# Performance work log

Measured on AMD Instinct MI355X. Metric: run time of the kernel, lower is better.

## Reference

```python
import jax, jax.numpy as jnp
import numpy as np
from jax import lax

B, C, H, W = 8, 128, 64, 64
S = 4          # patch_size
RED = 16       # SE reduction


def setup_inputs() -> dict:
    key = jax.random.key(0)
    ks = jax.random.split(key, 20)
    f = lambda k, shp, s=1.0: jax.random.normal(k, shp, dtype=jnp.float32) * s
    return {
        "F1": f(ks[0], (B, C, H // 2, W // 2)),
        "F2": f(ks[1], (B, C, H, W)),
        "F3": f(ks[2], (B, C, 2 * H, 2 * W)),
        "conv_w": f(ks[3], (3, C, C, 3, 3), 0.02),
        "conv_b": f(ks[4], (3, C), 0.02),
        "qw": f(ks[5], (3, C, C), 0.05), "qb": f(ks[6], (3, C), 0.02),
        "kw": f(ks[7], (3, C, C), 0.05), "kb": f(ks[8], (3, C), 0.02),
        "vw": f(ks[9], (3, C, C), 0.05), "vb": f(ks[10], (3, C), 0.02),
        "ca1_w": f(ks[11], (3 * C // RED, 3 * C), 0.05), "ca1_b": f(ks[12], (3 * C // RED,), 0.02),
        "ca2_w": f(ks[13], (3 * C, 3 * C // RED), 0.05), "ca2_b": f(ks[14], (3 * C,), 0.02),
        "c3d_w": f(ks[15], (C, C, 3), 0.05), "c3d_b": f(ks[16], (C,), 0.02),
        "out_w": f(ks[17], (C, C), 0.05), "out_b": f(ks[18], (C,), 0.02),
    }


def _conv3x3(x, w, b):
    y = lax.conv_general_dilated(x, w, (1, 1), 'SAME',
                                 dimension_numbers=('NCHW', 'OIHW', 'NCHW'))
    return y + b[None, :, None, None]


def _coarse_attn(x, qw, qb, kw, kb, vw, vb):
    # Block-coarse attention; A is block-constant so we never build HWxHW.
    b, c, h, w = x.shape
    hb, wb = h // S, w // S
    xb = x.reshape(b, c, hb, S, wb, S)
    x_avg = xb.mean((3, 5)).reshape(b, c, hb * wb).transpose(0, 2, 1)  # (B, Nb, C)
    Q = x_avg @ qw.T + qb
    K = x_avg @ kw.T + kb
    A = jax.nn.softmax(jnp.einsum('bnc,bmc->bnm', Q, K) / jnp.sqrt(jnp.float32(c)), axis=-1)
    V = x.transpose(0, 2, 3, 1).reshape(b, h * w, c) @ vw.T + vb       # (B, HW, C)
    Vb = V.reshape(b, hb, S, wb, S, c).sum((2, 4)).reshape(b, hb * wb, c)  # block-summed V
    ob = jnp.einsum('bnm,bmc->bnc', A, Vb)                             # (B, Nb, C)
    out = jnp.broadcast_to(ob.reshape(b, hb, 1, wb, 1, c), (b, hb, S, wb, S, c))
    return out.reshape(b, h, w, c).transpose(0, 3, 1, 2)


def reference(F1, F2, F3, conv_w, conv_b, qw, qb, kw, kb, vw, vb,
              ca1_w, ca1_b, ca2_w, ca2_b, c3d_w, c3d_b, out_w, out_b):
    bsz = F2.shape[0]
    # bilinear upsample (align_corners=False == half-pixel == jax.image.resize)
    F1u = jax.image.resize(F1, F2.shape, method='bilinear')
    # adaptive_avg_pool2d 2H,2W -> H,W is exact 2x2 mean pooling
    F3d = F3.reshape(bsz, C, H, 2, W, 2).mean((3, 5))
    ins = [F1u, F2, F3d]
    processed = [
        _conv3x3(ins[i], conv_w[i], conv_b[i])
        + _coarse_attn(ins[i], qw[i], qb[i], kw[i], kb[i], vw[i], vb[i])
        for i in range(3)
    ]
    cat = jnp.concatenate(processed, axis=1)  # (B, 3C, H, W)
    # SE channel attention
    y = cat.mean((2, 3))
    y = jax.nn.sigmoid(jax.nn.relu(y @ ca1_w.T + ca1_b) @ ca2_w.T + ca2_b)
    wf = cat * y[:, :, None, None]
    # conv3d (3,1,1) pad (1,0,0) then take depth index 1 == full contraction over depth
    stack = jnp.stack((wf[:, :C], wf[:, C:2 * C], wf[:, 2 * C:]), axis=2)  # (B, C, 3, H, W)
    mid = jnp.einsum('ocd,bcdhw->bohw', c3d_w, stack) + c3d_b[None, :, None, None]
    return jnp.einsum('oc,bchw->bohw', out_w, mid) + out_b[None, :, None, None]
```

## Files before the change

kernel.cpp:

```cpp
#include <hip/hip_runtime.h>
#include <hip/hip_bf16.h>
#include <cstddef>


typedef __bf16 bf16x8 __attribute__((ext_vector_type(8)));
typedef float f32x4 __attribute__((ext_vector_type(4)));

__device__ __forceinline__ unsigned short f2bf(float f) {
  unsigned int u = __float_as_uint(f);
  return (unsigned short)((u + 0x7fffu + ((u >> 16) & 1u)) >> 16);
}
__device__ __forceinline__ float bf2f(unsigned short h) {
  return __uint_as_float(((unsigned int)h) << 16);
}
__device__ __forceinline__ unsigned int packbf(float a, float b) {
  return (unsigned int)f2bf(a) | ((unsigned int)f2bf(b) << 16);
}

__global__ __launch_bounds__(256) void k_prep0(
    const float* __restrict__ conv_w, unsigned short* __restrict__ WG,
    const float* __restrict__ qw, const float* __restrict__ kw, const float* __restrict__ vw,
    float* __restrict__ qwT, float* __restrict__ kwT, float* __restrict__ vwT,
    const float* __restrict__ out_w, const float* __restrict__ c3d_w,
    float* __restrict__ comb2, const float* __restrict__ c3d_b,
    const float* __restrict__ out_b, float* __restrict__ fb,
    unsigned short* __restrict__ INS, float* __restrict__ ym,
    const float* __restrict__ F1, const float* __restrict__ F2,
    const float* __restrict__ F3) {
  int blk = blockIdx.x;
  int t = threadIdx.x;
  __shared__ alignas(16) unsigned short L[64 * 136];
  if (blk < 384) {
    int i = blk >> 7, co = blk & 127;
    float* Lw = (float*)L;
    const float* src = conv_w + (size_t)blk * 1152;
    for (int q = t; q < 1152; q += 256) Lw[q] = src[q];
    __syncthreads();
    for (int id = t; id < 576; id += 256) {
      int tap = id >> 6, cp = id & 63;
      int cc = cp >> 4, e = (cp & 15) * 2;
      unsigned int w = packbf(Lw[(cp * 2) * 9 + tap], Lw[(cp * 2 + 1) * 9 + tap]);
      *(unsigned int*)(WG + ((size_t)(((i * 9 + tap) * 4 + cc) * 128 + co)) * 32 + e) = w;
    }
    return;
  } else if (blk < 576) {
    int idx = (blk - 384) * 256 + t;
    int c = idx & 127, k = (idx >> 7) & 127, i = idx >> 14;
    int src = (i * 128 + c) * 128 + k;
    qwT[idx] = qw[src];
    kwT[idx] = kw[src];
    vwT[idx] = vw[src];
    return;
  } else if (blk < 768) {
    int idx = (blk - 576) * 256 + t;
    int j = idx % 384, o = idx / 384;
    int c = j & 127, d = j >> 7;
    float s = 0.f;
    for (int m = 0; m < 128; m++)
      s += out_w[o * 128 + m] * c3d_w[(m * 128 + c) * 3 + d];
    comb2[idx] = s;
    return;
  } else if (blk == 768) {
    if (t < 128) {
      float s = out_b[t];
      for (int m = 0; m < 128; m++) s += out_w[t * 128 + m] * c3d_b[m];
      fb[t] = s;
    }
    for (int z = t; z < 3072; z += 256) ym[z] = 0.f;
    return;
  } else if (blk < 793) {
    int ib = blk - 769;
    uint4 z = {0u, 0u, 0u, 0u};
    for (int id = t; id < 4160; id += 256) {
      int pxI = id >> 4, seg = id & 15;
      int yy, xxp;
      if (pxI < 66) { yy = 0; xxp = pxI; }
      else if (pxI < 132) { yy = 65; xxp = pxI - 66; }
      else if (pxI < 196) { yy = pxI - 131; xxp = 0; }
      else { yy = pxI - 195; xxp = 65; }
      *(uint4*)(INS + (((size_t)ib * 66 + yy) * 66 + xxp) * 128 + seg * 8) = z;
    }
    return;
  }
  int pidx = blk - 793;
  int y = pidx & 63, b = (pidx >> 6) & 7, i = pidx >> 9;
  int ib = i * 8 + b;
  if (i == 1) {
    int x = t & 63, cg = t >> 6;
    unsigned short* lrow = L + x * 136 + cg * 32;
    const float* src = F2 + (((size_t)b * 128 + cg * 32) * 64 + y) * 64 + x;
#pragma unroll 4
    for (int k = 0; k < 32; k += 2) {
      float a = src[(size_t)k * 4096];
      float c = src[(size_t)(k + 1) * 4096];
      *(unsigned int*)(lrow + k) = packbf(a, c);
    }
  } else if (i == 2) {
    int xp = t & 31, cg8 = t >> 5;
    const float* src = F3 + (((size_t)b * 128 + cg8 * 16) * 128 + 2 * y) * 128 + 4 * xp;
    unsigned short* l0 = L + (2 * xp) * 136 + cg8 * 16;
    unsigned short* l1 = L + (2 * xp + 1) * 136 + cg8 * 16;
#pragma unroll
    for (int k = 0; k < 16; ++k) {
      const float* p = src + (size_t)k * 16384;
      float4 a = *(const float4*)p;
      float4 c = *(const float4*)(p + 128);
      l0[k] = f2bf(0.25f * (a.x + a.y + c.x + c.y));
      l1[k] = f2bf(0.25f * (a.z + a.w + c.z + c.w));
    }
  } else {
    int x = t & 63, cg = t >> 6;
    unsigned short* lrow = L + x * 136 + cg * 32;
    int ky = y >> 1, kx = x >> 1;
    int y0, y1, x0, x1;
    float wy0, wx0;
    if (y & 1) { y0 = ky; y1 = (ky + 1 < 32) ? ky + 1 : 31; wy0 = 0.75f; }
    else       { y0 = (ky - 1 > 0) ? ky - 1 : 0; y1 = ky;   wy0 = 0.25f; }
    if (x & 1) { x0 = kx; x1 = (kx + 1 < 32) ? kx + 1 : 31; wx0 = 0.75f; }
    else       { x0 = (kx - 1 > 0) ? kx - 1 : 0; x1 = kx;   wx0 = 0.25f; }
    const float* base = F1 + ((size_t)b * 128 + cg * 32) * 1024;
#pragma unroll 4
    for (int k = 0; k < 32; k += 2) {
      float v[2];
#pragma unroll
      for (int kk = 0; kk < 2; ++kk) {
        const float* p = base + (size_t)(k + kk) * 1024;
        float top = wx0 * p[y0 * 32 + x0] + (1.f - wx0) * p[y0 * 32 + x1];
        float bot = wx0 * p[y1 * 32 + x0] + (1.f - wx0) * p[y1 * 32 + x1];
        v[kk] = wy0 * top + (1.f - wy0) * bot;
      }
      *(unsigned int*)(lrow + k) = packbf(v[0], v[1]);
    }
  }
  __syncthreads();
  unsigned short* dst = INS + (((size_t)ib * 66 + (y + 1)) * 66 + 1) * 128;
#pragma unroll
  for (int q = 0; q < 4; ++q) {
    int id = t + 256 * q;
    int xx = id >> 4, cseg = id & 15;
    uint4 v = *(const uint4*)(&L[xx * 136 + cseg * 8]);
    *(uint4*)(dst + (size_t)id * 8) = v;
  }
}

__global__ __launch_bounds__(256) void k_qkv(
    const unsigned short* __restrict__ INS,
    const float* __restrict__ qwT, const float* __restrict__ qb,
    const float* __restrict__ kwT, const float* __restrict__ kb,
    const float* __restrict__ vwT, const float* __restrict__ vb,
    unsigned short* __restrict__ Qb, unsigned short* __restrict__ Km,
    unsigned short* __restrict__ VT) {
  int nc = blockIdx.x, b = blockIdx.y, i = blockIdx.z;
  int ib = i * 8 + b;
  int t = threadIdx.x;
  __shared__ float xs[16 * 128];
  {
    int n = t >> 4, cs = t & 15;
    int gn = nc * 16 + n;
    int by = gn >> 4, bx = gn & 15;
    float acc[8];
#pragma unroll
    for (int e = 0; e < 8; ++e) acc[e] = 0.f;
#pragma unroll
    for (int ry = 0; ry < 4; ++ry) {
      int y = by * 4 + ry;
      const unsigned short* row = INS + (((size_t)ib * 66 + y + 1) * 66 + 1) * 128 + cs * 8;
#pragma unroll
      for (int rx = 0; rx < 4; ++rx) {
        int x = bx * 4 + rx;
        uint4 v0 = *(const uint4*)(row + (size_t)x * 128);
        unsigned int u[4] = {v0.x, v0.y, v0.z, v0.w};
#pragma unroll
        for (int q = 0; q < 4; ++q) {
          acc[2 * q] += bf2f((unsigned short)(u[q] & 0xffffu));
          acc[2 * q + 1] += bf2f((unsigned short)(u[q] >> 16));
        }
      }
    }
#pragma unroll
    for (int e = 0; e < 8; ++e) xs[n * 128 + cs * 8 + e] = acc[e] * (1.f / 16.f);
  }
  __syncthreads();
  int c = t & 127, nh = t >> 7;
  float aq[8], ak[8], av[8];
#pragma unroll
  for (int z = 0; z < 8; z++) { aq[z] = 0.f; ak[z] = 0.f; av[z] = 0.f; }
  for (int k = 0; k < 128; ++k) {
    float wq = qwT[(i * 128 + k) * 128 + c];
    float wk = kwT[(i * 128 + k) * 128 + c];
    float wv = vwT[(i * 128 + k) * 128 + c];
#pragma unroll
    for (int nn = 0; nn < 8; ++nn) {
      float xv = xs[(nh * 8 + nn) * 128 + k];
      aq[nn] += xv * wq; ak[nn] += xv * wk; av[nn] += xv * wv;
    }
  }
  float bq = qb[i * 128 + c], bk = kb[i * 128 + c], bv = vb[i * 128 + c];
  alignas(16) unsigned short vt[8];
#pragma unroll
  for (int nn = 0; nn < 8; ++nn) {
    size_t row = ((size_t)(ib * 256 + nc * 16 + nh * 8 + nn)) * 128 + c;
    Qb[row] = f2bf(aq[nn] + bq);
    Km[row] = f2bf(ak[nn] + bk);
    vt[nn] = f2bf(16.f * (av[nn] + bv));
  }
  *(uint4*)(VT + ((size_t)(ib * 128 + c)) * 256 + nc * 16 + nh * 8) = *(uint4*)vt;
}

__global__ __launch_bounds__(256) void k_attn(
    const unsigned short* __restrict__ Qb, const unsigned short* __restrict__ K,
    const unsigned short* __restrict__ VT, float* __restrict__ OB) {
  int nc = blockIdx.x, b = blockIdx.y, i = blockIdx.z;
  int ib = i * 8 + b;
  int qbase = nc * 16;
  int t = threadIdx.x;
  int w = t >> 6, l = t & 63;
  int lr = l & 15, lk = (l >> 4) * 8;
  __shared__ float Ss[16 * 260];
  __shared__ alignas(16) unsigned short Pb[16 * 280];

  const float SC = 0.08838834764831845f;
  {
    bf16x8 aq[4];
#pragma unroll
    for (int ks = 0; ks < 4; ++ks)
      aq[ks] = *(const bf16x8*)(Qb + ((size_t)(ib * 256 + qbase + lr)) * 128 + ks * 32 + lk);
    f32x4 acc[4];
#pragma unroll
    for (int nt = 0; nt < 4; ++nt) acc[nt] = {0.f, 0.f, 0.f, 0.f};
#pragma unroll
    for (int ks = 0; ks < 4; ++ks)
#pragma unroll
      for (int nt = 0; nt < 4; ++nt) {
        bf16x8 bk = *(const bf16x8*)(K + ((size_t)(ib * 256 + w * 64 + nt * 16 + lr)) * 128 + ks * 32 + lk);
        acc[nt] = __builtin_amdgcn_mfma_f32_16x16x32_bf16(aq[ks], bk, acc[nt], 0, 0, 0);
      }
#pragma unroll
    for (int nt = 0; nt < 4; ++nt)
#pragma unroll
      for (int r = 0; r < 4; ++r)
        Ss[((l >> 4) * 4 + r) * 260 + w * 64 + nt * 16 + lr] = acc[nt][r] * SC;
  }
  __syncthreads();
  {
    int n = t >> 4, ms = t & 15;
    float vals[16];
    float mx = -1e30f;
#pragma unroll
    for (int j = 0; j < 16; ++j) { vals[j] = Ss[n * 260 + ms + 16 * j]; mx = fmaxf(mx, vals[j]); }
    for (int d = 1; d < 16; d <<= 1) mx = fmaxf(mx, __shfl_xor(mx, d));
    float sum = 0.f;
#pragma unroll
    for (int j = 0; j < 16; ++j) { vals[j] = __expf(vals[j] - mx); sum += vals[j]; }
    for (int d = 1; d < 16; d <<= 1) sum += __shfl_xor(sum, d);
    float inv = 1.f / sum;
#pragma unroll
    for (int j = 0; j < 16; ++j) Pb[n * 280 + ms + 16 * j] = f2bf(vals[j] * inv);
  }
  __syncthreads();
  {
    f32x4 acc[2];
    acc[0] = {0.f, 0.f, 0.f, 0.f};
    acc[1] = acc[0];
#pragma unroll
    for (int ks = 0; ks < 8; ++ks) {
      bf16x8 ap = *(const bf16x8*)(&Pb[lr * 280 + ks * 32 + lk]);
#pragma unroll
      for (int nt = 0; nt < 2; ++nt) {
        bf16x8 bv = *(const bf16x8*)(VT + ((size_t)(ib * 128 + w * 32 + nt * 16 + lr)) * 256 + ks * 32 + lk);
        acc[nt] = __builtin_amdgcn_mfma_f32_16x16x32_bf16(ap, bv, acc[nt], 0, 0, 0);
      }
    }
#pragma unroll
    for (int nt = 0; nt < 2; ++nt)
#pragma unroll
      for (int r = 0; r < 4; ++r) {
        int q = (l >> 4) * 4 + r;
        int ch = w * 32 + nt * 16 + lr;
        OB[((size_t)(ib * 256 + qbase + q)) * 128 + ch] = acc[nt][r];
      }
  }
}

__global__ __launch_bounds__(256) void k_conv(
    const unsigned short* __restrict__ INS, const unsigned short* __restrict__ WG,
    const float* __restrict__ conv_b, const float* __restrict__ OB,
    unsigned short* __restrict__ catT, float* __restrict__ Ysum) {
  int yr = blockIdx.x;
  int yp = ((yr & 7) << 2) | (yr >> 3);
  int y0 = yp * 2;
  int b = blockIdx.y, i = blockIdx.z;
  int ib = i * 8 + b;
  int t = threadIdx.x;
  __shared__ alignas(16) unsigned short smem[17408];
  int w = t >> 6, l = t & 63;
  int lr = l & 15, q4 = l >> 4;

  f32x4 acc[2][2][4];
#pragma unroll
  for (int ro = 0; ro < 2; ++ro)
#pragma unroll
    for (int s = 0; s < 2; s++)
#pragma unroll
      for (int p = 0; p < 4; p++) acc[ro][s][p] = 0.f;

  auto stageX = [&](int h) {
    for (int cI = t; cI < 2112; cI += 256) {
      int seg = cI & 7, rj = cI >> 3;
      int r = rj / 66, j = rj - r * 66;
      uint4 v = *(const uint4*)(INS + (((size_t)ib * 66 + y0 + r) * 66 + j) * 128 + h * 64 + seg * 8);
      *(uint4*)(&smem[(r * 66 + j) * 64 + ((seg ^ (j & 7)) * 8)]) = v;
    }
  };

  const unsigned short* wbase = WG + (size_t)(i * 9) * 4 * 128 * 32 + (w * 32 + lr) * 32 + q4 * 8;
  auto wload = [&](bf16x8* dst, int s) {
    int tap = s % 9, cc = s / 9;
    const unsigned short* wp = wbase + (size_t)(tap * 4 + cc) * 4096;
    dst[0] = *(const bf16x8*)(wp);
    dst[1] = *(const bf16x8*)(wp + 16 * 32);
  };
  bf16x8 wbuf[3][2];
  stageX(0);
  wload(wbuf[0], 0);
  wload(wbuf[1], 1);
  __syncthreads();

#pragma unroll
  for (int s = 0; s < 36; ++s) {
    if (s + 2 < 36) wload(wbuf[(s + 2) % 3], s + 2);
    int tap = s % 9;
    int cc2 = (s / 9) & 1;
    int dy = tap / 3, dx = tap - dy * 3;
    int sid = cc2 * 4 + q4;
#pragma unroll
    for (int ro = 0; ro < 2; ++ro) {
      bf16x8 bfv[4];
#pragma unroll
      for (int p = 0; p < 4; ++p) {
        int j = p * 16 + lr + dx;
        bfv[p] = *(const bf16x8*)(&smem[((dy + ro) * 66 + j) * 64 + ((sid ^ (j & 7)) * 8)]);
      }
#pragma unroll
      for (int sf = 0; sf < 2; ++sf)
#pragma unroll
        for (int p = 0; p < 4; ++p)
          acc[ro][sf][p] = __builtin_amdgcn_mfma_f32_16x16x32_bf16(wbuf[s % 3][sf], bfv[p], acc[ro][sf][p], 0, 0, 0);
    }
    if (s == 17) {
      __syncthreads();
      stageX(1);
      __syncthreads();
    }
  }
  __syncthreads();

  unsigned short* Tt = smem;
  int cobase[2];
  cobase[0] = w * 32 + q4 * 4;
  cobase[1] = w * 32 + 16 + q4 * 4;
  float cb[2][4], ys[2][4];
#pragma unroll
  for (int sf = 0; sf < 2; ++sf)
#pragma unroll
    for (int q = 0; q < 4; ++q) {
      cb[sf][q] = conv_b[i * 128 + cobase[sf] + q];
      ys[sf][q] = 0.f;
    }
#pragma unroll
  for (int ro = 0; ro < 2; ++ro) {
    int nbase = ((y0 + ro) >> 2) * 16;
#pragma unroll
    for (int sf = 0; sf < 2; ++sf) {
#pragma unroll
      for (int p = 0; p < 4; ++p) {
        int px = p * 16 + lr;
        int n = nbase + (px >> 2);
        float4 obv = *(const float4*)(OB + ((size_t)(ib * 256 + n)) * 128 + cobase[sf]);
        float v0 = acc[ro][sf][p][0] + cb[sf][0] + obv.x;
        float v1 = acc[ro][sf][p][1] + cb[sf][1] + obv.y;
        float v2 = acc[ro][sf][p][2] + cb[sf][2] + obv.z;
        float v3 = acc[ro][sf][p][3] + cb[sf][3] + obv.w;
        ys[sf][0] += v0; ys[sf][1] += v1; ys[sf][2] += v2; ys[sf][3] += v3;
        int ploc = ro * 64 + px;
        *(unsigned int*)(&Tt[ploc * 136 + cobase[sf]]) = packbf(v0, v1);
        *(unsigned int*)(&Tt[ploc * 136 + cobase[sf] + 2]) = packbf(v2, v3);
      }
    }
  }
#pragma unroll
  for (int sf = 0; sf < 2; ++sf)
#pragma unroll
    for (int q = 0; q < 4; ++q) {
      float r = ys[sf][q];
      r += __shfl_xor(r, 1);
      r += __shfl_xor(r, 2);
      r += __shfl_xor(r, 4);
      r += __shfl_xor(r, 8);
      if (lr == 0) atomicAdd(&Ysum[b * 384 + i * 128 + cobase[sf] + q], r);
    }
  __syncthreads();
  for (int c2 = t; c2 < 2048; c2 += 256) {
    int ploc = c2 >> 4, seg = c2 & 15;
    uint4 v = *(const uint4*)(&Tt[ploc * 136 + seg * 8]);
    int yy = y0 + (ploc >> 6), xx = ploc & 63;
    *(uint4*)(catT + (((size_t)b * 4096) + yy * 64 + xx) * 384 + i * 128 + seg * 8) = v;
  }
}

__global__ __launch_bounds__(256) void k_final(
    const float* __restrict__ Ysum,
    const float* __restrict__ ca1_w, const float* __restrict__ ca1_b,
    const float* __restrict__ ca2_w, const float* __restrict__ ca2_b,
    const float* __restrict__ comb2, const unsigned short* __restrict__ catT,
    const float* __restrict__ fb, float* __restrict__ out) {
  int pc = blockIdx.x, b = blockIdx.y;
  int t = threadIdx.x;
  __shared__ alignas(16) unsigned short fsm[20480];
  __shared__ float ysh[384];
  __shared__ float sig[384];
  __shared__ float z1[24];
  unsigned short* Ab0 = fsm;
  unsigned short* Ab1 = fsm + 5120;
  unsigned short* Bb0 = fsm + 10240;
  unsigned short* Bb1 = fsm + 15360;

  int w = t >> 6, l = t & 63;
  int wo = w >> 1, wp = w & 1;
  int lr = l & 15, lk = (l >> 4) * 8;

  for (int j = t; j < 384; j += 256) ysh[j] = Ysum[b * 384 + j] * (1.f / 4096.f);
  __syncthreads();
  if (t < 24) {
    float s = ca1_b[t];
    for (int k = 0; k < 384; k++) s += ca1_w[t * 384 + k] * ysh[k];
    z1[t] = fmaxf(s, 0.f);
  }
  __syncthreads();
  for (int j = t; j < 384; j += 256) {
    float s = ca2_b[j];
#pragma unroll
    for (int k = 0; k < 24; k++) s += ca2_w[j * 24 + k] * z1[k];
    sig[j] = 1.f / (1.f + __expf(-s));
  }
  __syncthreads();

  f32x4 acc[4][4];
#pragma unroll
  for (int s = 0; s < 4; s++)
#pragma unroll
    for (int p = 0; p < 4; p++) acc[s][p] = 0.f;

  auto stageA = [&](unsigned short* Adst, int c) {
#pragma unroll
    for (int q = 0; q < 2; ++q) {
      int id = t + 256 * q;
      int o = id >> 2, seg = id & 3;
      int jb = c * 32 + seg * 8;
      const float* src = comb2 + (size_t)o * 384 + jb;
      float4 a = *(const float4*)src;
      float4 b4 = *(const float4*)(src + 4);
      alignas(16) unsigned short tmp[8];
      tmp[0] = f2bf(a.x * sig[jb + 0]);
      tmp[1] = f2bf(a.y * sig[jb + 1]);
      tmp[2] = f2bf(a.z * sig[jb + 2]);
      tmp[3] = f2bf(a.w * sig[jb + 3]);
      tmp[4] = f2bf(b4.x * sig[jb + 4]);
      tmp[5] = f2bf(b4.y * sig[jb + 5]);
      tmp[6] = f2bf(b4.z * sig[jb + 6]);
      tmp[7] = f2bf(b4.w * sig[jb + 7]);
      *(uint4*)(&Adst[o * 40 + seg * 8]) = *(uint4*)tmp;
    }
  };

  stageA(Ab0, 0);
  for (int q = 0; q < 2; ++q) {
    int id = t + 256 * q;
    int o = id >> 2, seg = id & 3;
    uint4 vb = *(const uint4*)(catT + ((size_t)b * 4096 + pc * 128 + o) * 384 + seg * 8);
    *(uint4*)(&Bb0[o * 40 + seg * 8]) = vb;
  }
  __syncthreads();

  for (int c = 0; c < 12; ++c) {
    unsigned short* Acur = (c & 1) ? Ab1 : Ab0;
    unsigned short* Bcur = (c & 1) ? Bb1 : Bb0;
    unsigned short* Anxt = (c & 1) ? Ab0 : Ab1;
    unsigned short* Bnxt = (c & 1) ? Bb0 : Bb1;
    uint4 bpf[2];
    if (c < 11) {
      stageA(Anxt, c + 1);
#pragma unroll
      for (int q = 0; q < 2; ++q) {
        int id = t + 256 * q;
        int o = id >> 2, seg = id & 3;
        bpf[q] = *(const uint4*)(catT + ((size_t)b * 4096 + pc * 128 + o) * 384 + (c + 1) * 32 + seg * 8);
      }
    }
    {
      bf16x8 af[4], bf_[4];
#pragma unroll
      for (int sf = 0; sf < 4; ++sf)
        af[sf] = *(const bf16x8*)(&Acur[(wo * 64 + sf * 16 + lr) * 40 + lk]);
#pragma unroll
      for (int p = 0; p < 4; ++p)
        bf_[p] = *(const bf16x8*)(&Bcur[(wp * 64 + p * 16 + lr) * 40 + lk]);
#pragma unroll
      for (int sf = 0; sf < 4; ++sf)
#pragma unroll
        for (int p = 0; p < 4; ++p)
          acc[sf][p] = __builtin_amdgcn_mfma_f32_16x16x32_bf16(af[sf], bf_[p], acc[sf][p], 0, 0, 0);
    }
    if (c < 11) {
#pragma unroll
      for (int q = 0; q < 2; ++q) {
        int id = t + 256 * q;
        int o = id >> 2, seg = id & 3;
        *(uint4*)(&Bnxt[o * 40 + seg * 8]) = bpf[q];
      }
    }
    __syncthreads();
  }

#pragma unroll
  for (int sf = 0; sf < 4; ++sf) {
    int obase = wo * 64 + sf * 16 + (l >> 4) * 4;
#pragma unroll
    for (int p = 0; p < 4; ++p) {
      int px = wp * 64 + p * 16 + lr;
#pragma unroll
      for (int q = 0; q < 4; ++q) {
        int o = obase + q;
        out[((size_t)(b * 128 + o)) * 4096 + pc * 128 + px] = acc[sf][p][q] + fb[o];
      }
    }
  }
}

extern "C" void kernel_launch(void* const* d_in, const int* in_sizes, int n_in,
                              void* d_out, int out_size, void* d_ws, size_t ws_size,
                              hipStream_t stream) {
  const float* F1 = (const float*)d_in[0];
  const float* F2 = (const float*)d_in[1];
  const float* F3 = (const float*)d_in[2];
  const float* conv_w = (const float*)d_in[3];
  const float* conv_b = (const float*)d_in[4];
  const float* qw = (const float*)d_in[5];
  const float* qb = (const float*)d_in[6];
  const float* kw = (const float*)d_in[7];
  const float* kb = (const float*)d_in[8];
  const float* vw = (const float*)d_in[9];
  const float* vb = (const float*)d_in[10];
  const float* ca1_w = (const float*)d_in[11];
  const float* ca1_b = (const float*)d_in[12];
  const float* ca2_w = (const float*)d_in[13];
  const float* ca2_b = (const float*)d_in[14];
  const float* c3d_w = (const float*)d_in[15];
  const float* c3d_b = (const float*)d_in[16];
  const float* out_w = (const float*)d_in[17];
  const float* out_b = (const float*)d_in[18];
  float* out = (float*)d_out;

  char* W = (char*)d_ws;
  unsigned short* INS  = (unsigned short*)W;
  unsigned short* CATT = (unsigned short*)(W + 26763264);
  unsigned short* QmB = (unsigned short*)(W + 51929088);
  unsigned short* KmB = (unsigned short*)(W + 55074816);
  unsigned short* VTB = (unsigned short*)(W + 58220544);
  float* OBm   = (float*)(W + 61366272);
  unsigned short* WG = (unsigned short*)(W + 64512000);
  float* QWT   = (float*)(W + 65396736);
  float* KWT   = (float*)(W + 65593344);
  float* VWT   = (float*)(W + 65789952);
  float* COMB2 = (float*)(W + 65986560);
  float* YM    = (float*)(W + 66183168);
  float* FB    = (float*)(W + 66195456);

  k_prep0<<<2329, 256, 0, stream>>>(conv_w, WG, qw, kw, vw, QWT, KWT, VWT,
                                    out_w, c3d_w, COMB2, c3d_b, out_b, FB, INS, YM,
                                    F1, F2, F3);
  k_qkv<<<dim3(16, 8, 3), 256, 0, stream>>>(INS, QWT, qb, KWT, kb, VWT, vb, QmB, KmB, VTB);
  k_attn<<<dim3(16, 8, 3), 256, 0, stream>>>(QmB, KmB, VTB, OBm);
  k_conv<<<dim3(32, 8, 3), 256, 0, stream>>>(INS, WG, conv_b, OBm, CATT, YM);
  k_final<<<dim3(32, 8), 256, 0, stream>>>(YM, ca1_w, ca1_b, ca2_w, ca2_b, COMB2, CATT, FB, out);
}
```

Measured before the change: 126.6 us.

## Use bf16 MFMA for QKV projection and deepen conv weight prefetch

The QKV projection kernel previously did scalar fp32 FMAs over transposed fp32 weights. It now converts the block means and the weights to bf16 and computes Q, K and V with 16x16x32 MFMA instructions, loading weights directly in their original layout. Separately, the conv kernel's weight register prefetch goes from a 3-deep to a 4-deep ring, with each load issued after the MFMAs that consume its slot. This trades some precision in the projections and extra registers in the conv kernel for less ALU work and better hiding of load latency.

New measurement: 116.5 us. 8.0% less time.

```diff
diff --git a/kernel.cpp b/kernel.cpp
--- a/kernel.cpp
+++ b/kernel.cpp
@@ -20,7 +20,8 @@
 __global__ __launch_bounds__(256) void k_prep0(
     const float* __restrict__ conv_w, unsigned short* __restrict__ WG,
     const float* __restrict__ qw, const float* __restrict__ kw, const float* __restrict__ vw,
-    float* __restrict__ qwT, float* __restrict__ kwT, float* __restrict__ vwT,
+    unsigned short* __restrict__ qwB, unsigned short* __restrict__ kwB,
+    unsigned short* __restrict__ vwB,
     const float* __restrict__ out_w, const float* __restrict__ c3d_w,
     float* __restrict__ comb2, const float* __restrict__ c3d_b,
     const float* __restrict__ out_b, float* __restrict__ fb,
@@ -45,11 +46,9 @@
     return;
   } else if (blk < 576) {
     int idx = (blk - 384) * 256 + t;
-    int c = idx & 127, k = (idx >> 7) & 127, i = idx >> 14;
-    int src = (i * 128 + c) * 128 + k;
-    qwT[idx] = qw[src];
-    kwT[idx] = kw[src];
-    vwT[idx] = vw[src];
+    qwB[idx] = f2bf(qw[idx]);
+    kwB[idx] = f2bf(kw[idx]);
+    vwB[idx] = f2bf(vw[idx]);
     return;
   } else if (blk < 768) {
     int idx = (blk - 576) * 256 + t;
@@ -145,18 +144,19 @@
 
 __global__ __launch_bounds__(256) void k_qkv(
     const unsigned short* __restrict__ INS,
-    const float* __restrict__ qwT, const float* __restrict__ qb,
-    const float* __restrict__ kwT, const float* __restrict__ kb,
-    const float* __restrict__ vwT, const float* __restrict__ vb,
+    const unsigned short* __restrict__ qwB, const float* __restrict__ qb,
+    const unsigned short* __restrict__ kwB, const float* __restrict__ kb,
+    const unsigned short* __restrict__ vwB, const float* __restrict__ vb,
     unsigned short* __restrict__ Qb, unsigned short* __restrict__ Km,
     unsigned short* __restrict__ VT) {
   int nc = blockIdx.x, b = blockIdx.y, i = blockIdx.z;
   int ib = i * 8 + b;
+  int qbase = nc * 16;
   int t = threadIdx.x;
-  __shared__ float xs[16 * 128];
+  __shared__ alignas(16) unsigned short xb[16 * 136];
   {
     int n = t >> 4, cs = t & 15;
-    int gn = nc * 16 + n;
+    int gn = qbase + n;
     int by = gn >> 4, bx = gn & 15;
     float acc[8];
 #pragma unroll
@@ -178,33 +178,50 @@
       }
     }
 #pragma unroll
-    for (int e = 0; e < 8; ++e) xs[n * 128 + cs * 8 + e] = acc[e] * (1.f / 16.f);
-  }
-  __syncthreads();
-  int c = t & 127, nh = t >> 7;
-  float aq[8], ak[8], av[8];
-#pragma unroll
-  for (int z = 0; z < 8; z++) { aq[z] = 0.f; ak[z] = 0.f; av[z] = 0.f; }
-  for (int k = 0; k < 128; ++k) {
-    float wq = qwT[(i * 128 + k) * 128 + c];
-    float wk = kwT[(i * 128 + k) * 128 + c];
-    float wv = vwT[(i * 128 + k) * 128 + c];
-#pragma unroll
-    for (int nn = 0; nn < 8; ++nn) {
-      float xv = xs[(nh * 8 + nn) * 128 + k];
-      aq[nn] += xv * wq; ak[nn] += xv * wk; av[nn] += xv * wv;
-    }
-  }
-  float bq = qb[i * 128 + c], bk = kb[i * 128 + c], bv = vb[i * 128 + c];
-  alignas(16) unsigned short vt[8];
-#pragma unroll
-  for (int nn = 0; nn < 8; ++nn) {
-    size_t row = ((size_t)(ib * 256 + nc * 16 + nh * 8 + nn)) * 128 + c;
-    Qb[row] = f2bf(aq[nn] + bq);
-    Km[row] = f2bf(ak[nn] + bk);
-    vt[nn] = f2bf(16.f * (av[nn] + bv));
-  }
-  *(uint4*)(VT + ((size_t)(ib * 128 + c)) * 256 + nc * 16 + nh * 8) = *(uint4*)vt;
+    for (int m = 0; m < 4; ++m)
+      *(unsigned int*)(&xb[n * 136 + cs * 8 + 2 * m]) =
+          packbf(acc[2 * m] * (1.f / 16.f), acc[2 * m + 1] * (1.f / 16.f));
+  }
+  __syncthreads();
+  int w = t >> 6, l = t & 63;
+  int lr = l & 15, lk = (l >> 4) * 8;
+  int cbase = w * 32;
+  bf16x8 ax[4];
+#pragma unroll
+  for (int ks = 0; ks < 4; ++ks)
+    ax[ks] = *(const bf16x8*)(&xb[lr * 136 + ks * 32 + lk]);
+
+#pragma unroll
+  for (int which = 0; which < 3; ++which) {
+    const unsigned short* wB = (which == 0) ? qwB : (which == 1) ? kwB : vwB;
+    const float* bias = (which == 0) ? qb : (which == 1) ? kb : vb;
+    f32x4 acc[2];
+    acc[0] = {0.f, 0.f, 0.f, 0.f};
+    acc[1] = acc[0];
+#pragma unroll
+    for (int ks = 0; ks < 4; ++ks)
+#pragma unroll
+      for (int nt = 0; nt < 2; ++nt) {
+        bf16x8 bw = *(const bf16x8*)(wB + ((size_t)(i * 128 + cbase + nt * 16 + lr)) * 128 + ks * 32 + lk);
+        acc[nt] = __builtin_amdgcn_mfma_f32_16x16x32_bf16(ax[ks], bw, acc[nt], 0, 0, 0);
+      }
+#pragma unroll
+    for (int nt = 0; nt < 2; ++nt) {
+      int c = cbase + nt * 16 + lr;
+      float bv = bias[i * 128 + c];
+#pragma unroll
+      for (int r = 0; r < 4; ++r) {
+        int n = (l >> 4) * 4 + r;
+        float v = acc[nt][r] + bv;
+        if (which == 0)
+          Qb[((size_t)(ib * 256 + qbase + n)) * 128 + c] = f2bf(v);
+        else if (which == 1)
+          Km[((size_t)(ib * 256 + qbase + n)) * 128 + c] = f2bf(v);
+        else
+          VT[((size_t)(ib * 128 + c)) * 256 + qbase + n] = f2bf(16.f * v);
+      }
+    }
+  }
 }
 
 __global__ __launch_bounds__(256) void k_attn(
@@ -320,15 +337,16 @@
     dst[0] = *(const bf16x8*)(wp);
     dst[1] = *(const bf16x8*)(wp + 16 * 32);
   };
-  bf16x8 wbuf[3][2];
+  bf16x8 wbuf[4][2];
   stageX(0);
   wload(wbuf[0], 0);
   wload(wbuf[1], 1);
+  wload(wbuf[2], 2);
+  wload(wbuf[3], 3);
   __syncthreads();
 
 #pragma unroll
   for (int s = 0; s < 36; ++s) {
-    if (s + 2 < 36) wload(wbuf[(s + 2) % 3], s + 2);
     int tap = s % 9;
     int cc2 = (s / 9) & 1;
     int dy = tap / 3, dx = tap - dy * 3;
@@ -345,8 +363,9 @@
       for (int sf = 0; sf < 2; ++sf)
 #pragma unroll
         for (int p = 0; p < 4; ++p)
-          acc[ro][sf][p] = __builtin_amdgcn_mfma_f32_16x16x32_bf16(wbuf[s % 3][sf], bfv[p], acc[ro][sf][p], 0, 0, 0);
-    }
+          acc[ro][sf][p] = __builtin_amdgcn_mfma_f32_16x16x32_bf16(wbuf[s & 3][sf], bfv[p], acc[ro][sf][p], 0, 0, 0);
+    }
+    if (s + 4 < 36) wload(wbuf[s & 3], s + 4);
     if (s == 17) {
       __syncthreads();
       stageX(1);
@@ -569,17 +588,17 @@
   unsigned short* VTB = (unsigned short*)(W + 58220544);
   float* OBm   = (float*)(W + 61366272);
   unsigned short* WG = (unsigned short*)(W + 64512000);
-  float* QWT   = (float*)(W + 65396736);
-  float* KWT   = (float*)(W + 65593344);
-  float* VWT   = (float*)(W + 65789952);
+  unsigned short* QWB = (unsigned short*)(W + 65396736);
+  unsigned short* KWB = (unsigned short*)(W + 65593344);
+  unsigned short* VWB = (unsigned short*)(W + 65789952);
   float* COMB2 = (float*)(W + 65986560);
   float* YM    = (float*)(W + 66183168);
   float* FB    = (float*)(W + 66195456);
 
-  k_prep0<<<2329, 256, 0, stream>>>(conv_w, WG, qw, kw, vw, QWT, KWT, VWT,
+  k_prep0<<<2329, 256, 0, stream>>>(conv_w, WG, qw, kw, vw, QWB, KWB, VWB,
                                     out_w, c3d_w, COMB2, c3d_b, out_b, FB, INS, YM,
                                     F1, F2, F3);
-  k_qkv<<<dim3(16, 8, 3), 256, 0, stream>>>(INS, QWT, qb, KWT, kb, VWT, vb, QmB, KmB, VTB);
+  k_qkv<<<dim3(16, 8, 3), 256, 0, stream>>>(INS, QWB, qb, KWB, kb, VWB, vb, QmB, KmB, VTB);
   k_attn<<<dim3(16, 8, 3), 256, 0, stream>>>(QmB, KmB, VTB, OBm);
   k_conv<<<dim3(32, 8, 3), 256, 0, stream>>>(INS, WG, conv_b, OBm, CATT, YM);
   k_final<<<dim3(32, 8), 256, 0, stream>>>(YM, ca1_w, ca1_b, ca2_w, ca2_b, COMB2, CATT, FB, out);
```
